# Kernel optimization log

Hardware: AMD Instinct MI355X
Metric: run time of the kernel (lower is better)

The kernel has to match this reference:

```python
import jax, jax.numpy as jnp
import numpy as np

N_EMBD = 500
BLOCK_SIZE = 256


def _rope(q, k, theta=0.0001):
    # Faithful to the torch code: freq exponent uses the FULL dim C, and the
    # tensor is split into contiguous halves (not interleaved pairs).
    B, T, C = q.shape
    half = C // 2
    i = jnp.arange(half)
    freqs = theta ** (2.0 * (i // 2).astype(q.dtype) / C)  # [half]
    ang = jnp.arange(T, dtype=q.dtype)[:, None] * freqs[None, :]  # [T, half]
    cos_p, sin_p = jnp.cos(ang), jnp.sin(ang)
    q1, q2 = q[..., :half], q[..., half:]
    k1, k2 = k[..., :half], k[..., half:]
    q_rot = jnp.concatenate([q1 * cos_p - q2 * sin_p, q1 * sin_p + q2 * cos_p], axis=-1)
    k_rot = jnp.concatenate([k1 * cos_p - k2 * sin_p, k1 * sin_p + k2 * cos_p], axis=-1)
    return q_rot, k_rot


def setup_inputs() -> dict:
    key = jax.random.key(0)
    k1, k2, k3, k4 = jax.random.split(key, 4)
    B, T = 256, 256
    scale = 1.0 / np.sqrt(N_EMBD)
    x = jax.random.normal(k1, (B, T, N_EMBD), dtype=jnp.float32)
    Wq = jax.random.normal(k2, (N_EMBD, 500), dtype=jnp.float32) * scale
    Wk = jax.random.normal(k3, (N_EMBD, 500), dtype=jnp.float32) * scale
    Wv = jax.random.normal(k4, (N_EMBD, 500), dtype=jnp.float32) * scale
    return {"x": x, "Wq": Wq, "Wk": Wk, "Wv": Wv}


def reference(x, Wq, Wk, Wv):
    B, T, C = x.shape  # C == n_embd == 500
    q = jnp.einsum("btc,ch->bth", x, Wq)
    k = jnp.einsum("btc,ch->bth", x, Wk)
    q, k = _rope(q, k)
    # NOTE: original scales by input-dim C**-0.5 (500), not head_size**-0.5.
    wei = jnp.einsum("bth,bsh->bts", q, k) * (C ** -0.5)
    causal = jnp.tril(jnp.ones((T, T), dtype=bool))
    wei = jnp.where(causal, wei, -jnp.inf)
    wei = jax.nn.softmax(wei, axis=-1)
    # dropout: eval mode (identity) for deterministic reference
    v = jnp.einsum("btc,ch->bth", x, Wv)
    return jnp.einsum("bts,bsh->bth", wei, v)
```

## Files before the change

### kernel.cpp

```cpp
#include <hip/hip_runtime.h>

typedef unsigned short u16;
typedef __attribute__((ext_vector_type(8))) __bf16 bf16x8;
typedef __attribute__((ext_vector_type(4))) float f32x4;

__device__ __forceinline__ float bf2f(u16 u) {
  union { unsigned int i; float f; } v; v.i = ((unsigned int)u) << 16; return v.f;
}
__device__ __forceinline__ u16 f2bf(float f) {
  union { float f; unsigned int i; } v; v.f = f;
  unsigned int u = v.i;
  return (u16)((u + 0x7fffu + ((u >> 16) & 1u)) >> 16);
}
__device__ __forceinline__ void async16(void* lds, const void* g) {
  __builtin_amdgcn_global_load_lds(
      (const __attribute__((address_space(1))) unsigned int*)g,
      (__attribute__((address_space(3))) unsigned int*)lds, 16, 0, 0);
}

__global__ void k_convert_x(const float* __restrict__ x, u16* __restrict__ xb) {
  int idx = blockIdx.x * 256 + threadIdx.x;
  int m = idx >> 6, c0 = (idx & 63) * 8;
  u16 o[8];
#pragma unroll
  for (int j = 0; j < 8; ++j) {
    int c = c0 + j;
    o[j] = f2bf((c < 500) ? x[(size_t)m * 500 + c] : 0.f);
  }
  *(uint4*)(xb + (size_t)m * 512 + c0) = *(const uint4*)o;
}

__global__ void k_convert_w(const float* __restrict__ Wq, const float* __restrict__ Wk,
                            const float* __restrict__ Wv, u16* __restrict__ Wt) {
  int idx = blockIdx.x * 256 + threadIdx.x;
  int g = idx >> 18;
  int r = idx & 262143;
  int n = r >> 9, k = r & 511;
  const float* W = (g == 0) ? Wq : (g == 1) ? Wk : Wv;
  int orig = (g == 2) ? n : ((n & 1) ? (n >> 1) + 250 : (n >> 1));
  float v = (n < 500 && k < 500) ? W[(size_t)k * 500 + orig] : 0.f;
  Wt[idx] = f2bf(v);
}

__global__ void k_tables(float* __restrict__ cospair, float* __restrict__ sinpair) {
  int t = blockIdx.x, p = threadIdx.x;
  float c = 0.f, s = 0.f;
  if (p < 250) {
    float ex = (float)(2 * (p >> 1)) / 500.0f;
    float fr = powf(1e-4f, ex);
    float ang = (float)t * fr;
    c = cosf(ang); s = sinf(ang);
  }
  cospair[t * 256 + p] = c;
  sinpair[t * 256 + p] = s;
}

__global__ __launch_bounds__(256, 2) void k_gemm_qkv(
    const u16* __restrict__ xb, const u16* __restrict__ Wt,
    const float* __restrict__ cospair, const float* __restrict__ sinpair,
    u16* __restrict__ qb, u16* __restrict__ kb, u16* __restrict__ vT) {
  __shared__ u16 As[4][128][64];
  const int tid = threadIdx.x;
  const int lane = tid & 63;
  const int w = tid >> 6;
  const int wm = w >> 1, wn = w & 1;
  const int lrow = lane & 15, lhi = lane >> 4;
  const int sx = lrow & 7;

  int bid = blockIdx.x;
  int wk = (bid & 7) * 384 + (bid >> 3);
  int mg = wk / 24;
  int j24 = wk - mg * 24;
  int g = j24 >> 3, bni = j24 & 7;
  const int bn = bni << 6;
  const int m0 = mg << 9;

  const u16* Ab = xb + (size_t)m0 * 512;

  bf16x8 breg[8][2][2];
  {
    const u16* Bl = Wt + ((size_t)(g * 512 + bn + wn * 32) + lrow) * 512 + lhi * 8;
#pragma unroll
    for (int t = 0; t < 8; ++t)
#pragma unroll
      for (int ni = 0; ni < 2; ++ni)
#pragma unroll
        for (int kk2 = 0; kk2 < 2; ++kk2)
          breg[t][ni][kk2] =
              *(const bf16x8*)(Bl + (size_t)ni * 16 * 512 + t * 64 + kk2 * 32);
  }

#define STAGE(S) { int mt_ = (S) >> 3, t_ = (S) & 7, buf_ = (S) & 3;          \
    _Pragma("unroll")                                                         \
    for (int ld = 0; ld < 4; ++ld) {                                          \
      int gi = ld * 256 + tid;                                                \
      int r_ = gi >> 3, c_ = gi & 7;                                          \
      async16((char*)As + buf_ * 16384 + (size_t)gi * 16,                     \
              Ab + ((size_t)(mt_ * 128 + r_)) * 512 + t_ * 64 +               \
                  ((c_ ^ (r_ & 7)) * 8));                                     \
    } }

#define COMPUTE(S, T) {                                                       \
    const u16* Asl = (const u16*)As + ((S) & 3) * 8192;                       \
    bf16x8 a[4][2];                                                           \
    _Pragma("unroll")                                                         \
    for (int mi = 0; mi < 4; ++mi)                                            \
      _Pragma("unroll")                                                       \
      for (int kk2 = 0; kk2 < 2; ++kk2)                                       \
        a[mi][kk2] = *(const bf16x8*)(Asl + (wm * 64 + mi * 16 + lrow) * 64 + \
                                      (((kk2 * 4 + lhi) ^ sx) * 8));          \
    __builtin_amdgcn_s_setprio(1);                                            \
    _Pragma("unroll")                                                         \
    for (int kk2 = 0; kk2 < 2; ++kk2)                                         \
      _Pragma("unroll")                                                       \
      for (int mi = 0; mi < 4; ++mi)                                          \
        _Pragma("unroll")                                                     \
        for (int ni = 0; ni < 2; ++ni)                                        \
          acc[mi][ni] = __builtin_amdgcn_mfma_f32_16x16x32_bf16(              \
              a[mi][kk2], breg[T][ni][kk2], acc[mi][ni], 0, 0, 0);            \
    __builtin_amdgcn_s_setprio(0);                                            \
  }

#define EPILOGUE(MT) {                                                        \
    int mb = m0 + (MT) * 128;                                                 \
    if (g < 2) {                                                              \
      u16* dst = (g == 0) ? qb : kb;                                          \
      _Pragma("unroll")                                                       \
      for (int mi = 0; mi < 4; ++mi)                                          \
        _Pragma("unroll")                                                     \
        for (int ni = 0; ni < 2; ++ni) {                                      \
          int n = bn + wn * 32 + ni * 16 + lrow;                              \
          int p = n >> 1;                                                     \
          _Pragma("unroll")                                                   \
          for (int jj = 0; jj < 4; ++jj) {                                    \
            int m = mb + wm * 64 + mi * 16 + lhi * 4 + jj;                    \
            float v = acc[mi][ni][jj];                                        \
            float o = __shfl_xor(v, 1, 64);                                   \
            int ti = (m & 255) * 256 + p;                                     \
            float c = cospair[ti], s = sinpair[ti];                           \
            float r = (n & 1) ? (o * s + v * c) : (v * c - o * s);            \
            dst[(size_t)m * 512 + n] = f2bf(r);                               \
          }                                                                   \
        }                                                                     \
    } else {                                                                  \
      _Pragma("unroll")                                                       \
      for (int mi = 0; mi < 4; ++mi)                                          \
        _Pragma("unroll")                                                     \
        for (int ni = 0; ni < 2; ++ni) {                                      \
          int n = bn + wn * 32 + ni * 16 + lrow;                              \
          _Pragma("unroll")                                                   \
          for (int jj = 0; jj < 4; ++jj) {                                    \
            int m = mb + wm * 64 + mi * 16 + lhi * 4 + jj;                    \
            vT[(size_t)(m >> 8) * 131072 + (size_t)n * 256 + (m & 255)] =     \
                f2bf(acc[mi][ni][jj]);                                        \
          }                                                                   \
        }                                                                     \
    } }

#define PHASE(S, C)                                                           \
    STAGE((S) + 2); STAGE((S) + 3);                                           \
    COMPUTE((S), C); COMPUTE((S) + 1, C + 1);                                 \
    asm volatile("s_waitcnt vmcnt(0)" ::: "memory");                          \
    __builtin_amdgcn_s_barrier();                                             \
    asm volatile("" ::: "memory");

  STAGE(0); STAGE(1);
  asm volatile("s_waitcnt vmcnt(0)" ::: "memory");
  __builtin_amdgcn_s_barrier();
  asm volatile("" ::: "memory");

  for (int mt = 0; mt < 3; ++mt) {
    f32x4 acc[4][2] = {};
    const int S0 = mt * 8;
    PHASE(S0 + 0, 0)
    PHASE(S0 + 2, 2)
    PHASE(S0 + 4, 4)
    PHASE(S0 + 6, 6)
    EPILOGUE(mt);
  }
  {
    f32x4 acc[4][2] = {};
    PHASE(24, 0)
    PHASE(26, 2)
    STAGE(30); STAGE(31);
    COMPUTE(28, 4); COMPUTE(29, 5);
    asm volatile("s_waitcnt vmcnt(0)" ::: "memory");
    __builtin_amdgcn_s_barrier();
    asm volatile("" ::: "memory");
    COMPUTE(30, 6); COMPUTE(31, 7);
    EPILOGUE(3);
  }
#undef STAGE
#undef COMPUTE
#undef EPILOGUE
#undef PHASE
}

__global__ __launch_bounds__(256) void k_attn(
    const u16* __restrict__ qb, const u16* __restrict__ kb,
    const u16* __restrict__ vT, float* __restrict__ out) {
  __shared__ u16 smem[40960];
  u16* Ring = smem;
  u16* Ps = smem + 24576;

  const int tid = threadIdx.x;
  const int lane = tid & 63;
  const int w = tid >> 6;
  int bid = blockIdx.x;
  int wkk = (bid & 7) * 128 + (bid >> 3);
  const int b = wkk >> 2;
  const int qt = wkk & 3;
  const int t0 = qt * 64;
  const int lrow = lane & 15, lhi = lane >> 4;
  const int sx = lrow & 7;
  const int vxor = (lrow >> 1) & 3;
  const int NT = 4 * (qt + 1);
  const int NTB = 2 * (qt + 1);
  const int NV = 2 * NTB;

  const u16* qrow = qb + ((size_t)(b * 256 + t0 + w * 16 + lrow)) * 512;
  bf16x8 qf[16];
#pragma unroll
  for (int kk = 0; kk < 16; ++kk)
    qf[kk] = *(const bf16x8*)(qrow + kk * 32 + lhi * 8);

#define STAGE_K(ST) {                                                         \
    _Pragma("unroll")                                                         \
    for (int ld = 0; ld < 4; ++ld) {                                          \
      int gi = ld * 256 + tid;                                                \
      int r_ = gi >> 6, c_ = gi & 63;                                         \
      async16((char*)Ring + ((ST) % 3) * 16384 + (size_t)gi * 16,             \
              kb + ((size_t)(b * 256 + (ST) * 16 + r_)) * 512 +               \
                  ((c_ ^ (r_ & 7)) * 8));                                     \
    } }

#define STAGE_V(ST, HH) {                                                     \
    _Pragma("unroll")                                                         \
    for (int ld = 0; ld < 4; ++ld) {                                          \
      int gi = ld * 256 + tid;                                                \
      int r_ = gi >> 2, c_ = gi & 3;                                          \
      async16((char*)Ring + (((ST) * 2 + (HH)) % 3) * 16384 + (size_t)gi * 16,\
              vT + (size_t)b * 131072 + ((size_t)((HH) * 256 + r_)) * 256 +   \
                  (ST) * 32 + ((c_ ^ ((r_ >> 1) & 3)) * 8));                  \
    } }

  f32x4 sa[16] = {};
  STAGE_K(0); STAGE_K(1);
  asm volatile("s_waitcnt vmcnt(4)" ::: "memory");
  __builtin_amdgcn_s_barrier();
  asm volatile("" ::: "memory");
#pragma unroll
  for (int st = 0; st < 16; ++st) {
    if (st < NT) {
      if (st + 2 < NT) STAGE_K(st + 2);
      const u16* Ksl = Ring + (st % 3) * 8192 + lrow * 512;
      __builtin_amdgcn_s_setprio(1);
#pragma unroll
      for (int kk = 0; kk < 16; ++kk) {
        bf16x8 bf = *(const bf16x8*)(Ksl + ((kk * 4 + lhi) ^ sx) * 8);
        sa[st] = __builtin_amdgcn_mfma_f32_16x16x32_bf16(qf[kk], bf, sa[st], 0, 0, 0);
      }
      __builtin_amdgcn_s_setprio(0);
      if (st + 2 < NT)      asm volatile("s_waitcnt vmcnt(4)" ::: "memory");
      else if (st + 1 < NT) asm volatile("s_waitcnt vmcnt(0)" ::: "memory");
      if (st + 1 < NT) {
        __builtin_amdgcn_s_barrier();
        asm volatile("" ::: "memory");
      }
    }
  }

  const float scale = 0.04472135954999579f;
  float rmax[4] = {-1e30f, -1e30f, -1e30f, -1e30f};
#pragma unroll
  for (int n = 0; n < 16; ++n) {
    int s = n * 16 + lrow;
#pragma unroll
    for (int j = 0; j < 4; ++j) {
      int t = t0 + w * 16 + lhi * 4 + j;
      float v = sa[n][j] * scale;
      if (s > t) v = -1e30f;
      sa[n][j] = v;
      rmax[j] = fmaxf(rmax[j], v);
    }
  }
#pragma unroll
  for (int j = 0; j < 4; ++j)
#pragma unroll
    for (int msk = 1; msk < 16; msk <<= 1)
      rmax[j] = fmaxf(rmax[j], __shfl_xor(rmax[j], msk, 64));
  float rsum[4] = {0.f, 0.f, 0.f, 0.f};
#pragma unroll
  for (int n = 0; n < 16; ++n)
#pragma unroll
    for (int j = 0; j < 4; ++j) {
      float p = __expf(sa[n][j] - rmax[j]);
      sa[n][j] = p;
      rsum[j] += p;
    }
#pragma unroll
  for (int j = 0; j < 4; ++j)
#pragma unroll
    for (int msk = 1; msk < 16; msk <<= 1)
      rsum[j] += __shfl_xor(rsum[j], msk, 64);
  float rinv[4];
#pragma unroll
  for (int j = 0; j < 4; ++j) rinv[j] = 1.0f / rsum[j];

#pragma unroll
  for (int n = 0; n < 16; ++n)
#pragma unroll
    for (int j = 0; j < 4; ++j) {
      int s = n * 16 + lrow;
      int trow = w * 16 + lhi * 4 + j;
      int slot = (s >> 3) ^ (trow & 7);
      Ps[trow * 256 + slot * 8 + (s & 7)] = f2bf(sa[n][j] * rinv[j]);
    }

  __syncthreads();

  f32x4 o[2][16] = {};
  STAGE_V(0, 0); STAGE_V(0, 1);
  asm volatile("s_waitcnt vmcnt(4)" ::: "memory");
  __builtin_amdgcn_s_barrier();
  asm volatile("" ::: "memory");
#pragma unroll
  for (int st = 0; st < 8; ++st) {
    if (st < NTB) {
#pragma unroll
      for (int hh = 0; hh < 2; ++hh) {
        const int f = st * 2 + hh;
        if (f + 2 < NV) {
          if (hh == 0) STAGE_V(st + 1, 0) else STAGE_V(st + 1, 1);
        }
        bf16x8 pf = *(const bf16x8*)&Ps[(w * 16 + lrow) * 256 + ((st * 4 + lhi) ^ sx) * 8];
        const u16* Vsl = Ring + (f % 3) * 8192;
        __builtin_amdgcn_s_setprio(1);
#pragma unroll
        for (int ni = 0; ni < 16; ++ni) {
          bf16x8 vf = *(const bf16x8*)(Vsl + (ni * 16 + lrow) * 32 + (lhi ^ vxor) * 8);
          o[hh][ni] = __builtin_amdgcn_mfma_f32_16x16x32_bf16(pf, vf, o[hh][ni], 0, 0, 0);
        }
        __builtin_amdgcn_s_setprio(0);
        if (f + 2 < NV)      asm volatile("s_waitcnt vmcnt(4)" ::: "memory");
        else if (f + 1 < NV) asm volatile("s_waitcnt vmcnt(0)" ::: "memory");
        if (f + 1 < NV) {
          __builtin_amdgcn_s_barrier();
          asm volatile("" ::: "memory");
        }
      }
    }
  }
#undef STAGE_K
#undef STAGE_V

  const int tb = t0 + w * 16;
#pragma unroll
  for (int hh = 0; hh < 2; ++hh)
#pragma unroll
    for (int ni = 0; ni < 16; ++ni) {
      int h = hh * 256 + ni * 16 + lrow;
      if (h < 500) {
#pragma unroll
        for (int j = 0; j < 4; ++j) {
          int t = tb + lhi * 4 + j;
          out[((size_t)(b * 256 + t)) * 500 + h] = o[hh][ni][j];
        }
      }
    }
}

extern "C" void kernel_launch(void* const* d_in, const int* in_sizes, int n_in,
                              void* d_out, int out_size, void* d_ws, size_t ws_size,
                              hipStream_t stream) {
  const float* x  = (const float*)d_in[0];
  const float* Wq = (const float*)d_in[1];
  const float* Wk = (const float*)d_in[2];
  const float* Wv = (const float*)d_in[3];
  float* out = (float*)d_out;

  u16* xb = (u16*)d_ws;
  u16* qb = xb + 33554432;
  u16* kb = qb + 33554432;
  u16* vT = kb + 33554432;
  u16* Wt = vT + 33554432;
  float* cospair = (float*)(Wt + 786432);
  float* sinpair = cospair + 65536;

  k_convert_x<<<16384, 256, 0, stream>>>(x, xb);
  k_convert_w<<<3072, 256, 0, stream>>>(Wq, Wk, Wv, Wt);
  k_tables<<<256, 256, 0, stream>>>(cospair, sinpair);
  k_gemm_qkv<<<3072, 256, 0, stream>>>(xb, Wt, cospair, sinpair, qb, kb, vT);
  k_attn<<<1024, 256, 0, stream>>>(qb, kb, vT, out);
}
```

Baseline: 353.1 us.

## Stream weight fragments through double-buffered registers instead of preloading all

The QKV projection kernel no longer holds all 32 weight fragments in registers for the whole block. It now loads two k-steps of B fragments per phase into alternating register buffers and overlaps those loads with the A-tile async copies, using partial vmcnt waits. This frees many VGPRs, which may raise occupancy or ease register pressure. In exchange, weight fragments are reloaded from global memory (mostly L2) for every m-tile, and the ordering of the vmcnt counts is more fragile.

```diff
diff --git a/kernel.cpp b/kernel.cpp
--- a/kernel.cpp
+++ b/kernel.cpp
@@ -76,19 +76,9 @@
   const int m0 = mg << 9;
 
   const u16* Ab = xb + (size_t)m0 * 512;
-
-  bf16x8 breg[8][2][2];
-  {
-    const u16* Bl = Wt + ((size_t)(g * 512 + bn + wn * 32) + lrow) * 512 + lhi * 8;
-#pragma unroll
-    for (int t = 0; t < 8; ++t)
-#pragma unroll
-      for (int ni = 0; ni < 2; ++ni)
-#pragma unroll
-        for (int kk2 = 0; kk2 < 2; ++kk2)
-          breg[t][ni][kk2] =
-              *(const bf16x8*)(Bl + (size_t)ni * 16 * 512 + t * 64 + kk2 * 32);
-  }
+  const u16* Bl = Wt + ((size_t)(g * 512 + bn + wn * 32) + lrow) * 512 + lhi * 8;
+
+  bf16x8 bA[8], bB[8];
 
 #define STAGE(S) { int mt_ = (S) >> 3, t_ = (S) & 7, buf_ = (S) & 3;          \
     _Pragma("unroll")                                                         \
@@ -100,7 +90,18 @@
                   ((c_ ^ (r_ & 7)) * 8));                                     \
     } }
 
-#define COMPUTE(S, T) {                                                       \
+#define BLOAD(BUF, C) {                                                       \
+    _Pragma("unroll")                                                         \
+    for (int ni = 0; ni < 2; ++ni)                                            \
+      _Pragma("unroll")                                                       \
+      for (int kk2 = 0; kk2 < 2; ++kk2) {                                     \
+        BUF[ni * 2 + kk2] =                                                   \
+            *(const bf16x8*)(Bl + (size_t)ni * 16 * 512 + (C) * 64 + kk2 * 32);\
+        BUF[4 + ni * 2 + kk2] =                                               \
+            *(const bf16x8*)(Bl + (size_t)ni * 16 * 512 + ((C) + 1) * 64 + kk2 * 32);\
+      } }
+
+#define COMPUTE(S, H, BUF) {                                                  \
     const u16* Asl = (const u16*)As + ((S) & 3) * 8192;                       \
     bf16x8 a[4][2];                                                           \
     _Pragma("unroll")                                                         \
@@ -117,7 +118,7 @@
         _Pragma("unroll")                                                     \
         for (int ni = 0; ni < 2; ++ni)                                        \
           acc[mi][ni] = __builtin_amdgcn_mfma_f32_16x16x32_bf16(              \
-              a[mi][kk2], breg[T][ni][kk2], acc[mi][ni], 0, 0, 0);            \
+              a[mi][kk2], BUF[(H) * 4 + ni * 2 + kk2], acc[mi][ni], 0, 0, 0); \
     __builtin_amdgcn_s_setprio(0);                                            \
   }
 
@@ -157,43 +158,59 @@
         }                                                                     \
     } }
 
-#define PHASE(S, C)                                                           \
+#define PHASE(S, C, CUR, NXT)                                                 \
     STAGE((S) + 2); STAGE((S) + 3);                                           \
-    COMPUTE((S), C); COMPUTE((S) + 1, C + 1);                                 \
-    asm volatile("s_waitcnt vmcnt(0)" ::: "memory");                          \
+    asm volatile("" ::: "memory");                                            \
+    BLOAD(NXT, (((C) + 2) & 7));                                              \
+    asm volatile("s_waitcnt vmcnt(16)" ::: "memory");                         \
+    COMPUTE((S), 0, CUR); COMPUTE((S) + 1, 1, CUR);                           \
+    asm volatile("s_waitcnt vmcnt(8)" ::: "memory");                          \
     __builtin_amdgcn_s_barrier();                                             \
     asm volatile("" ::: "memory");
 
   STAGE(0); STAGE(1);
-  asm volatile("s_waitcnt vmcnt(0)" ::: "memory");
+  asm volatile("" ::: "memory");
+  BLOAD(bA, 0);
+  asm volatile("s_waitcnt vmcnt(8)" ::: "memory");
   __builtin_amdgcn_s_barrier();
   asm volatile("" ::: "memory");
 
-  for (int mt = 0; mt < 3; ++mt) {
-    f32x4 acc[4][2] = {};
-    const int S0 = mt * 8;
-    PHASE(S0 + 0, 0)
-    PHASE(S0 + 2, 2)
-    PHASE(S0 + 4, 4)
-    PHASE(S0 + 6, 6)
-    EPILOGUE(mt);
-  }
+#define MT_FULL(MT)                                                           \
+  {                                                                           \
+    f32x4 acc[4][2] = {};                                                     \
+    PHASE((MT) * 8 + 0, 0, bA, bB)                                            \
+    PHASE((MT) * 8 + 2, 2, bB, bA)                                            \
+    PHASE((MT) * 8 + 4, 4, bA, bB)                                            \
+    PHASE((MT) * 8 + 6, 6, bB, bA)                                            \
+    EPILOGUE(MT);                                                             \
+    asm volatile("s_waitcnt vmcnt(0)" ::: "memory");                          \
+  }
+
+  MT_FULL(0)
+  MT_FULL(1)
+  MT_FULL(2)
   {
     f32x4 acc[4][2] = {};
-    PHASE(24, 0)
-    PHASE(26, 2)
+    PHASE(24, 0, bA, bB)
+    PHASE(26, 2, bB, bA)
     STAGE(30); STAGE(31);
-    COMPUTE(28, 4); COMPUTE(29, 5);
-    asm volatile("s_waitcnt vmcnt(0)" ::: "memory");
+    asm volatile("" ::: "memory");
+    BLOAD(bB, 6);
+    asm volatile("s_waitcnt vmcnt(16)" ::: "memory");
+    COMPUTE(28, 0, bA); COMPUTE(29, 1, bA);
+    asm volatile("s_waitcnt vmcnt(8)" ::: "memory");
     __builtin_amdgcn_s_barrier();
     asm volatile("" ::: "memory");
-    COMPUTE(30, 6); COMPUTE(31, 7);
+    asm volatile("s_waitcnt vmcnt(0)" ::: "memory");
+    COMPUTE(30, 0, bB); COMPUTE(31, 1, bB);
     EPILOGUE(3);
   }
 #undef STAGE
+#undef BLOAD
 #undef COMPUTE
 #undef EPILOGUE
 #undef PHASE
+#undef MT_FULL
 }
 
 __global__ __launch_bounds__(256) void k_attn(
```

New measurement: 453.6 us. 28.5% more time.
